# Kernel optimization log

Measured on AMD Instinct MI355X. Metric: run time of the kernel, lower is better.

## Reference

```python
import jax, jax.numpy as jnp
import numpy as np
from jax import lax

B, T, I, H = 64, 784, 1, 600


def setup_inputs() -> dict:
    key = jax.random.key(0)
    ks = jax.random.split(key, 9)
    k = 1.0 / np.sqrt(H)  # pytorch LSTMCell/Linear init scale
    x = jax.random.normal(ks[0], (B, T, I), dtype=jnp.float32)
    hs0 = jax.random.normal(ks[1], (B, H), dtype=jnp.float32)
    cs0 = jax.random.normal(ks[2], (B, H), dtype=jnp.float32)
    W_ih = jax.random.normal(ks[3], (4 * H, I), dtype=jnp.float32) * k
    W_hh = jax.random.normal(ks[4], (4 * H, H), dtype=jnp.float32) * k
    b_ih = jax.random.normal(ks[5], (4 * H,), dtype=jnp.float32) * k
    b_hh = jax.random.normal(ks[6], (4 * H,), dtype=jnp.float32) * k
    W_out = jax.random.normal(ks[7], (10, H), dtype=jnp.float32) * k
    b_out = jax.random.normal(ks[8], (10,), dtype=jnp.float32) * k
    return {"x": x, "hs0": hs0, "cs0": cs0, "W_ih": W_ih, "W_hh": W_hh,
            "b_ih": b_ih, "b_hh": b_hh, "W_out": W_out, "b_out": b_out}


def reference(x, hs0, cs0, W_ih, W_hh, b_ih, b_hh, W_out, b_out):
    # Precompute input projections for all timesteps in one GEMM: [B,T,4H]
    pre = jnp.einsum('bti,gi->btg', x, W_ih) + b_ih + b_hh
    pre_t = jnp.swapaxes(pre, 0, 1)  # [T,B,4H]

    def step(carry, p):
        h, c = carry
        gates = p + h @ W_hh.T  # [B,4H], pytorch gate order i,f,g,o
        i, f, g, o = jnp.split(gates, 4, axis=-1)
        c = jax.nn.sigmoid(f) * c + jax.nn.sigmoid(i) * jnp.tanh(g)
        h = jax.nn.sigmoid(o) * jnp.tanh(c)
        return (h, c), None

    (h, _), _ = lax.scan(step, (hs0, cs0), pre_t)
    return h @ W_out.T + b_out  # [B,10]
```

## Files before the change

kernel.cpp:

```cpp
#include <hip/hip_runtime.h>
#include <math.h>

#define BB 64
#define TT 784
#define HH 600
#define CG 50
#define SGN 4
#define CPW 12
#define BW 16
#define NWG (CG*SGN)
#define BLOCK 512
#define HB4 (BW*150)
#define LDS_BYTES (84*1024)

typedef float f2v __attribute__((ext_vector_type(2)));

__device__ __forceinline__ void ldg5_bypass(const float4* g0, const float4* g1,
                                            const float4* g2, const float4* g3,
                                            const float4* g4,
                                            float4& a, float4& b, float4& c,
                                            float4& d, float4& e) {
    asm volatile(
        "global_load_dwordx4 %0, %5, off sc0 sc1\n\t"
        "global_load_dwordx4 %1, %6, off sc0 sc1\n\t"
        "global_load_dwordx4 %2, %7, off sc0 sc1\n\t"
        "global_load_dwordx4 %3, %8, off sc0 sc1\n\t"
        "global_load_dwordx4 %4, %9, off sc0 sc1\n\t"
        "s_waitcnt vmcnt(0)"
        : "=&v"(a), "=&v"(b), "=&v"(c), "=&v"(d), "=&v"(e)
        : "v"(g0), "v"(g1), "v"(g2), "v"(g3), "v"(g4)
        : "memory");
}

__device__ __forceinline__ void stg_bypass(float* p, float v) {
    asm volatile("global_store_dword %0, %1, off sc0 sc1"
                 :: "v"(p), "v"(v) : "memory");
}

__device__ __forceinline__ float sigm_f(float v) {
    return 1.f / (1.f + __expf(-v));
}
__device__ __forceinline__ float tanh_f(float v) {
    return 1.f - 2.f / (__expf(2.f * v) + 1.f);
}

template<int MASK, int CNT>
__device__ __forceinline__ void fold(float* v, int kh) {
    const bool hi = (kh & MASK) != 0;
    #pragma unroll
    for (int i = 0; i < CNT; ++i) {
        float send = hi ? v[i] : v[i + CNT];
        float recv = __shfl_xor(send, MASK);
        v[i] = (hi ? v[i + CNT] : v[i]) + recv;
    }
}

extern "C" __global__ void __launch_bounds__(BLOCK, 2)
lstm_main(const float* __restrict__ x, const float* __restrict__ hs0,
          const float* __restrict__ cs0, const float* __restrict__ W_ih,
          const float* __restrict__ W_hh, const float* __restrict__ b_ih,
          const float* __restrict__ b_hh, float* __restrict__ hbuf,
          unsigned int* __restrict__ flags)
{
    extern __shared__ float lds[];
    float4* h4l  = (float4*)lds;
    float*  g_lds = lds + 4 * HB4;

    const int wg   = blockIdx.x;
    const int cg   = wg % CG;
    const int sg   = wg / CG;
    const int tid  = threadIdx.x;
    const int w    = tid >> 6;
    const int lane = tid & 63;
    const int bh   = lane >> 5;
    const int kh   = lane & 31;
    const int khc  = (kh < 30) ? kh : 29;
    const int b0   = sg * BW;

    f2v Wr2[6][10];
    #pragma unroll
    for (int r = 0; r < 6; ++r) {
        const int row = 6 * w + r;
        const int g   = row / 12, c = row % 12;
        const float* wrow = W_hh + ((size_t)g * HH + cg * CPW + c) * HH + khc * 20;
        #pragma unroll
        for (int j = 0; j < 5; ++j) {
            float4 t4 = (kh < 30) ? *(const float4*)(wrow + 4 * j)
                                  : make_float4(0.f, 0.f, 0.f, 0.f);
            Wr2[r][2 * j]     = (f2v){t4.x, t4.y};
            Wr2[r][2 * j + 1] = (f2v){t4.z, t4.w};
        }
    }

    float wihv[4], biasv[4], cst = 0.f;
    const int pc = tid >> 4, pb = tid & 15;
    const int cell = cg * CPW + pc;
    const int bglob = b0 + pb;
    if (tid < 192) {
        #pragma unroll
        for (int g = 0; g < 4; ++g) {
            const int grow = g * HH + cell;
            wihv[g]  = W_ih[grow];
            biasv[g] = b_ih[grow] + b_hh[grow];
        }
        cst = cs0[(size_t)bglob * HH + cell];
    }

    const int i0 = tid, i1 = tid + 512, i2 = tid + 1024, i3 = tid + 1536;
    const int i4 = (tid + 2048 < HB4) ? tid + 2048 : HB4 - 1;

    unsigned int* myflag = &flags[wg * 16];

    for (int t = 0; t < TT; ++t) {
        float xv = 0.f;
        if (tid < 192) xv = x[(size_t)bglob * TT + t];

        if (t > 0) {
            if (tid < CG) {
                const unsigned int* f = &flags[(sg * CG + tid) * 16];
                while (__hip_atomic_load(f, __ATOMIC_RELAXED,
                                         __HIP_MEMORY_SCOPE_AGENT) < (unsigned)t)
                    __builtin_amdgcn_s_sleep(1);
            }
        }
        __syncthreads();

        {
            const float* hsrc = (t == 0) ? hs0 : (hbuf + (size_t)(t & 1) * BB * HH);
            const float4* s4 = (const float4*)hsrc + (size_t)b0 * 150;
            float4 v0, v1, v2, v3, v4;
            ldg5_bypass(s4 + i0, s4 + i1, s4 + i2, s4 + i3, s4 + i4,
                        v0, v1, v2, v3, v4);
            h4l[i0] = v0; h4l[i1] = v1; h4l[i2] = v2; h4l[i3] = v3; h4l[i4] = v4;
        }
        __syncthreads();

        float v[48];
        {
            f2v acc2[6][8];
            #pragma unroll
            for (int r = 0; r < 6; ++r)
                #pragma unroll
                for (int bi = 0; bi < 8; ++bi)
                    acc2[r][bi] = (f2v){0.f, 0.f};

            const float4* hb_base = h4l + (size_t)bh * 8 * 150 + khc * 5;
            #pragma unroll
            for (int bi = 0; bi < 8; ++bi) {
                const float4* hb = hb_base + bi * 150;
                float4 hv[5];
                hv[0] = hb[0]; hv[1] = hb[1]; hv[2] = hb[2];
                hv[3] = hb[3]; hv[4] = hb[4];
                const f2v* h2 = (const f2v*)hv;
                #pragma unroll
                for (int r = 0; r < 6; ++r)
                    #pragma unroll
                    for (int j = 0; j < 10; ++j)
                        acc2[r][bi] = __builtin_elementwise_fma(Wr2[r][j],
                                                                h2[j],
                                                                acc2[r][bi]);
            }
            #pragma unroll
            for (int r = 0; r < 6; ++r)
                #pragma unroll
                for (int bi = 0; bi < 8; ++bi)
                    v[r * 8 + bi] = acc2[r][bi][0] + acc2[r][bi][1];
        }

        fold<16, 24>(v, kh);
        fold<8, 12>(v, kh);
        fold<4, 6>(v, kh);
        fold<2, 3>(v, kh);
        #pragma unroll
        for (int i = 0; i < 3; ++i)
            v[i] += __shfl_xor(v[i], 1);

        if (!(kh & 1)) {
            const int vb = 3 * (kh >> 1);
            #pragma unroll
            for (int s = 0; s < 3; ++s) {
                const int val = vb + s;
                const int rowl = val >> 3, bi = val & 7;
                g_lds[(6 * w + rowl) * 16 + bh * 8 + bi] = v[s];
            }
        }
        __syncthreads();

        float* hdst = hbuf + (size_t)((t + 1) & 1) * BB * HH;
        if (tid < 192) {
            const float gi = g_lds[(0 * 12 + pc) * 16 + pb] + xv * wihv[0] + biasv[0];
            const float gf = g_lds[(1 * 12 + pc) * 16 + pb] + xv * wihv[1] + biasv[1];
            const float gg = g_lds[(2 * 12 + pc) * 16 + pb] + xv * wihv[2] + biasv[2];
            const float go = g_lds[(3 * 12 + pc) * 16 + pb] + xv * wihv[3] + biasv[3];
            const float cn = sigm_f(gf) * cst + sigm_f(gi) * tanh_f(gg);
            cst = cn;
            stg_bypass(&hdst[(size_t)bglob * HH + cell], sigm_f(go) * tanh_f(cn));
        }
        asm volatile("s_waitcnt vmcnt(0)" ::: "memory");
        __syncthreads();
        if (tid == 0)
            __hip_atomic_store(myflag, (unsigned)(t + 1), __ATOMIC_RELAXED,
                               __HIP_MEMORY_SCOPE_AGENT);
    }
}

extern "C" __global__ void lstm_out(const float* __restrict__ hbuf0,
                                    const float* __restrict__ W_out,
                                    const float* __restrict__ b_out,
                                    float* __restrict__ out)
{
    int b = blockIdx.x;
    int lane = threadIdx.x;
    float acc[10] = {};
    for (int k = lane; k < HH; k += 64) {
        float hv = hbuf0[(size_t)b * HH + k];
        #pragma unroll
        for (int o = 0; o < 10; ++o)
            acc[o] += hv * W_out[(size_t)o * HH + k];
    }
    #pragma unroll
    for (int o = 0; o < 10; ++o) {
        float v = acc[o];
        for (int off = 32; off > 0; off >>= 1) v += __shfl_down(v, off);
        if (lane == 0) out[b * 10 + o] = v + b_out[o];
    }
}

extern "C" void kernel_launch(void* const* d_in, const int* in_sizes, int n_in,
                              void* d_out, int out_size, void* d_ws, size_t ws_size,
                              hipStream_t stream)
{
    const float* x     = (const float*)d_in[0];
    const float* hs0   = (const float*)d_in[1];
    const float* cs0   = (const float*)d_in[2];
    const float* W_ih  = (const float*)d_in[3];
    const float* W_hh  = (const float*)d_in[4];
    const float* b_ih  = (const float*)d_in[5];
    const float* b_hh  = (const float*)d_in[6];
    const float* W_out = (const float*)d_in[7];
    const float* b_out = (const float*)d_in[8];
    float* out = (float*)d_out;

    float* hbuf = (float*)d_ws;
    unsigned int* flags = (unsigned int*)((char*)d_ws + (size_t)2 * BB * HH * sizeof(float));

    hipFuncSetAttribute((const void*)lstm_main,
                        hipFuncAttributeMaxDynamicSharedMemorySize, LDS_BYTES);

    hipMemsetAsync(flags, 0, NWG * 16 * sizeof(unsigned int), stream);
    hipLaunchKernelGGL(lstm_main, dim3(NWG), dim3(BLOCK), LDS_BYTES, stream,
                       x, hs0, cs0, W_ih, W_hh, b_ih, b_hh, hbuf, flags);
    hipLaunchKernelGGL(lstm_out, dim3(BB), dim3(64), 0, stream,
                       hbuf, W_out, b_out, out);
}
```

Measured before the change: 4.499 ms.

## Split K across waves with per-wave flag polling and async global-to-LDS h chunks

Moves W_hh from registers into LDS and splits the hidden dimension across the 8 waves. Each wave waits only on the producer workgroups whose h columns it consumes, then streams those chunks straight into LDS with global_load_lds and computes as each chunk lands. The shuffle-based reduction tree is replaced by LDS atomicAdd into the gate buffer. Flags become counters bumped by three waves per step, which removes the block-wide wait before the whole-h copy. The cost is more LDS traffic for weights, LDS atomic contention, and a lower occupancy hint.

```diff
diff --git a/kernel.cpp b/kernel.cpp
--- a/kernel.cpp
+++ b/kernel.cpp
@@ -5,31 +5,22 @@
 #define TT 784
 #define HH 600
 #define CG 50
-#define SGN 4
 #define CPW 12
 #define BW 16
-#define NWG (CG*SGN)
+#define NWG (CG*4)
 #define BLOCK 512
-#define HB4 (BW*150)
-#define LDS_BYTES (84*1024)
+#define WSTR 612
+#define CBUF_DW 192
+#define NBUF 7
+#define LDS_BYTES ((48*WSTR + 8*NBUF*CBUF_DW + 48*16)*4)
 
 typedef float f2v __attribute__((ext_vector_type(2)));
 
-__device__ __forceinline__ void ldg5_bypass(const float4* g0, const float4* g1,
-                                            const float4* g2, const float4* g3,
-                                            const float4* g4,
-                                            float4& a, float4& b, float4& c,
-                                            float4& d, float4& e) {
-    asm volatile(
-        "global_load_dwordx4 %0, %5, off sc0 sc1\n\t"
-        "global_load_dwordx4 %1, %6, off sc0 sc1\n\t"
-        "global_load_dwordx4 %2, %7, off sc0 sc1\n\t"
-        "global_load_dwordx4 %3, %8, off sc0 sc1\n\t"
-        "global_load_dwordx4 %4, %9, off sc0 sc1\n\t"
-        "s_waitcnt vmcnt(0)"
-        : "=&v"(a), "=&v"(b), "=&v"(c), "=&v"(d), "=&v"(e)
-        : "v"(g0), "v"(g1), "v"(g2), "v"(g3), "v"(g4)
-        : "memory");
+__device__ __forceinline__ float sigm_f(float v) {
+    return 1.f / (1.f + __expf(-v));
+}
+__device__ __forceinline__ float tanh_f(float v) {
+    return 1.f - 2.f / (__expf(2.f * v) + 1.f);
 }
 
 __device__ __forceinline__ void stg_bypass(float* p, float v) {
@@ -37,25 +28,43 @@
                  :: "v"(p), "v"(v) : "memory");
 }
 
-__device__ __forceinline__ float sigm_f(float v) {
-    return 1.f / (1.f + __expf(-v));
-}
-__device__ __forceinline__ float tanh_f(float v) {
-    return 1.f - 2.f / (__expf(2.f * v) + 1.f);
-}
-
-template<int MASK, int CNT>
-__device__ __forceinline__ void fold(float* v, int kh) {
-    const bool hi = (kh & MASK) != 0;
+template<int NCH>
+__device__ __forceinline__ void process_chunks(const float* __restrict__ W_lds,
+                                               const float* __restrict__ mycbuf,
+                                               int nst, int rt, int bt,
+                                               f2v (&acc2)[3][4])
+{
     #pragma unroll
-    for (int i = 0; i < CNT; ++i) {
-        float send = hi ? v[i] : v[i + CNT];
-        float recv = __shfl_xor(send, MASK);
-        v[i] = (hi ? v[i + CNT] : v[i]) + recv;
-    }
-}
-
-extern "C" __global__ void __launch_bounds__(BLOCK, 2)
+    for (int i = 0; i < NCH; ++i) {
+        asm volatile("s_waitcnt vmcnt(%c0)" :: "n"(NCH - 1 - i) : "memory");
+        __builtin_amdgcn_sched_barrier(0);
+        const float* cb = mycbuf + i * CBUF_DW;
+        float4 hv[4][3];
+        #pragma unroll
+        for (int jj = 0; jj < 4; ++jj)
+            #pragma unroll
+            for (int jc = 0; jc < 3; ++jc)
+                hv[jj][jc] = *(const float4*)&cb[(3 * (4 * bt + jj) + jc) * 4];
+        const int p = nst + i;
+        #pragma unroll
+        for (int ii = 0; ii < 3; ++ii) {
+            const float* wrow = W_lds + (3 * rt + ii) * WSTR + 12 * p;
+            #pragma unroll
+            for (int jc = 0; jc < 3; ++jc) {
+                float4 wv = *(const float4*)&wrow[4 * jc];
+                const f2v* w2 = (const f2v*)&wv;
+                #pragma unroll
+                for (int jj = 0; jj < 4; ++jj) {
+                    const f2v* h2 = (const f2v*)&hv[jj][jc];
+                    acc2[ii][jj] = __builtin_elementwise_fma(w2[0], h2[0], acc2[ii][jj]);
+                    acc2[ii][jj] = __builtin_elementwise_fma(w2[1], h2[1], acc2[ii][jj]);
+                }
+            }
+        }
+    }
+}
+
+extern "C" __global__ void __launch_bounds__(BLOCK)
 lstm_main(const float* __restrict__ x, const float* __restrict__ hs0,
           const float* __restrict__ cs0, const float* __restrict__ W_ih,
           const float* __restrict__ W_hh, const float* __restrict__ b_ih,
@@ -63,8 +72,9 @@
           unsigned int* __restrict__ flags)
 {
     extern __shared__ float lds[];
-    float4* h4l  = (float4*)lds;
-    float*  g_lds = lds + 4 * HB4;
+    float* W_lds = lds;
+    float* cbuf  = lds + 48 * WSTR;
+    float* g_lds = lds + 48 * WSTR + 8 * NBUF * CBUF_DW;
 
     const int wg   = blockIdx.x;
     const int cg   = wg % CG;
@@ -72,30 +82,26 @@
     const int tid  = threadIdx.x;
     const int w    = tid >> 6;
     const int lane = tid & 63;
-    const int bh   = lane >> 5;
-    const int kh   = lane & 31;
-    const int khc  = (kh < 30) ? kh : 29;
+    const int rt   = lane >> 2;
+    const int bt   = lane & 3;
     const int b0   = sg * BW;
-
-    f2v Wr2[6][10];
-    #pragma unroll
-    for (int r = 0; r < 6; ++r) {
-        const int row = 6 * w + r;
-        const int g   = row / 12, c = row % 12;
-        const float* wrow = W_hh + ((size_t)g * HH + cg * CPW + c) * HH + khc * 20;
-        #pragma unroll
-        for (int j = 0; j < 5; ++j) {
-            float4 t4 = (kh < 30) ? *(const float4*)(wrow + 4 * j)
-                                  : make_float4(0.f, 0.f, 0.f, 0.f);
-            Wr2[r][2 * j]     = (f2v){t4.x, t4.y};
-            Wr2[r][2 * j + 1] = (f2v){t4.z, t4.w};
-        }
-    }
-
-    float wihv[4], biasv[4], cst = 0.f;
+    const int nst  = (25 * w) >> 2;
+    const int nen  = (25 * (w + 1)) >> 2;
+    const int nch  = nen - nst;
+    const int sb   = lane / 3, sj = lane - 3 * sb;
+    float* mycbuf  = cbuf + w * NBUF * CBUF_DW;
+
+    for (int i4 = tid; i4 < 48 * 150; i4 += BLOCK) {
+        int r = i4 / 150, col = i4 - r * 150;
+        int gg = r / 12, cc = r - gg * 12;
+        *(float4*)&W_lds[r * WSTR + 4 * col] =
+            *(const float4*)(W_hh + ((size_t)(gg * HH + cg * CPW + cc)) * HH + 4 * col);
+    }
+
     const int pc = tid >> 4, pb = tid & 15;
     const int cell = cg * CPW + pc;
     const int bglob = b0 + pb;
+    float wihv[4], biasv[4], cst = 0.f;
     if (tid < 192) {
         #pragma unroll
         for (int g = 0; g < 4; ++g) {
@@ -106,101 +112,65 @@
         cst = cs0[(size_t)bglob * HH + cell];
     }
 
-    const int i0 = tid, i1 = tid + 512, i2 = tid + 1024, i3 = tid + 1536;
-    const int i4 = (tid + 2048 < HB4) ? tid + 2048 : HB4 - 1;
-
     unsigned int* myflag = &flags[wg * 16];
+    const unsigned int* pollp =
+        &flags[(sg * CG + nst + ((lane < nch) ? lane : 0)) * 16];
+    const bool mine = (lane < nch);
 
     for (int t = 0; t < TT; ++t) {
-        float xv = 0.f;
-        if (tid < 192) xv = x[(size_t)bglob * TT + t];
+        if (tid < 192) *(float4*)&g_lds[4 * tid] = make_float4(0.f, 0.f, 0.f, 0.f);
+        __syncthreads();
 
         if (t > 0) {
-            if (tid < CG) {
-                const unsigned int* f = &flags[(sg * CG + tid) * 16];
-                while (__hip_atomic_load(f, __ATOMIC_RELAXED,
-                                         __HIP_MEMORY_SCOPE_AGENT) < (unsigned)t)
-                    __builtin_amdgcn_s_sleep(1);
+            const unsigned thr3 = 3u * (unsigned)t;
+            for (;;) {
+                unsigned fv = __hip_atomic_load(pollp, __ATOMIC_RELAXED,
+                                                __HIP_MEMORY_SCOPE_AGENT);
+                if (__all(!mine || fv >= thr3)) break;
+                __builtin_amdgcn_s_sleep(1);
             }
         }
+        const float* hsrc = (t == 0) ? hs0 : (hbuf + (size_t)(t & 1) * BB * HH);
+        for (int i = 0; i < nch; ++i) {
+            if (lane < 48) {
+                const float* gp = hsrc + (size_t)(b0 + sb) * HH
+                                       + 12 * (nst + i) + 4 * sj;
+                __builtin_amdgcn_global_load_lds(gp, (void*)(mycbuf + i * CBUF_DW),
+                                                 16, 0, 17 );
+            }
+        }
+        f2v acc2[3][4];
+        #pragma unroll
+        for (int ii = 0; ii < 3; ++ii)
+            #pragma unroll
+            for (int jj = 0; jj < 4; ++jj)
+                acc2[ii][jj] = (f2v){0.f, 0.f};
+        if (nch == 7) process_chunks<7>(W_lds, mycbuf, nst, rt, bt, acc2);
+        else          process_chunks<6>(W_lds, mycbuf, nst, rt, bt, acc2);
+
+        #pragma unroll
+        for (int ii = 0; ii < 3; ++ii)
+            #pragma unroll
+            for (int jj = 0; jj < 4; ++jj)
+                atomicAdd(&g_lds[(3 * rt + ii) * 16 + 4 * bt + jj],
+                          acc2[ii][jj][0] + acc2[ii][jj][1]);
         __syncthreads();
 
-        {
-            const float* hsrc = (t == 0) ? hs0 : (hbuf + (size_t)(t & 1) * BB * HH);
-            const float4* s4 = (const float4*)hsrc + (size_t)b0 * 150;
-            float4 v0, v1, v2, v3, v4;
-            ldg5_bypass(s4 + i0, s4 + i1, s4 + i2, s4 + i3, s4 + i4,
-                        v0, v1, v2, v3, v4);
-            h4l[i0] = v0; h4l[i1] = v1; h4l[i2] = v2; h4l[i3] = v3; h4l[i4] = v4;
+        if (tid < 192) {
+            const float xv = x[(size_t)bglob * TT + t];
+            const float gi  = g_lds[(0 * CPW + pc) * 16 + pb] + xv * wihv[0] + biasv[0];
+            const float gf  = g_lds[(1 * CPW + pc) * 16 + pb] + xv * wihv[1] + biasv[1];
+            const float gg_ = g_lds[(2 * CPW + pc) * 16 + pb] + xv * wihv[2] + biasv[2];
+            const float go  = g_lds[(3 * CPW + pc) * 16 + pb] + xv * wihv[3] + biasv[3];
+            const float cn = sigm_f(gf) * cst + sigm_f(gi) * tanh_f(gg_);
+            cst = cn;
+            const float hv = sigm_f(go) * tanh_f(cn);
+            stg_bypass(hbuf + (size_t)((t + 1) & 1) * BB * HH
+                            + (size_t)bglob * HH + cell, hv);
+            asm volatile("s_waitcnt vmcnt(0)" ::: "memory");
+            if (lane == 0) atomicAdd(myflag, 1u);
         }
         __syncthreads();
-
-        float v[48];
-        {
-            f2v acc2[6][8];
-            #pragma unroll
-            for (int r = 0; r < 6; ++r)
-                #pragma unroll
-                for (int bi = 0; bi < 8; ++bi)
-                    acc2[r][bi] = (f2v){0.f, 0.f};
-
-            const float4* hb_base = h4l + (size_t)bh * 8 * 150 + khc * 5;
-            #pragma unroll
-            for (int bi = 0; bi < 8; ++bi) {
-                const float4* hb = hb_base + bi * 150;
-                float4 hv[5];
-                hv[0] = hb[0]; hv[1] = hb[1]; hv[2] = hb[2];
-                hv[3] = hb[3]; hv[4] = hb[4];
-                const f2v* h2 = (const f2v*)hv;
-                #pragma unroll
-                for (int r = 0; r < 6; ++r)
-                    #pragma unroll
-                    for (int j = 0; j < 10; ++j)
-                        acc2[r][bi] = __builtin_elementwise_fma(Wr2[r][j],
-                                                                h2[j],
-                                                                acc2[r][bi]);
-            }
-            #pragma unroll
-            for (int r = 0; r < 6; ++r)
-                #pragma unroll
-                for (int bi = 0; bi < 8; ++bi)
-                    v[r * 8 + bi] = acc2[r][bi][0] + acc2[r][bi][1];
-        }
-
-        fold<16, 24>(v, kh);
-        fold<8, 12>(v, kh);
-        fold<4, 6>(v, kh);
-        fold<2, 3>(v, kh);
-        #pragma unroll
-        for (int i = 0; i < 3; ++i)
-            v[i] += __shfl_xor(v[i], 1);
-
-        if (!(kh & 1)) {
-            const int vb = 3 * (kh >> 1);
-            #pragma unroll
-            for (int s = 0; s < 3; ++s) {
-                const int val = vb + s;
-                const int rowl = val >> 3, bi = val & 7;
-                g_lds[(6 * w + rowl) * 16 + bh * 8 + bi] = v[s];
-            }
-        }
-        __syncthreads();
-
-        float* hdst = hbuf + (size_t)((t + 1) & 1) * BB * HH;
-        if (tid < 192) {
-            const float gi = g_lds[(0 * 12 + pc) * 16 + pb] + xv * wihv[0] + biasv[0];
-            const float gf = g_lds[(1 * 12 + pc) * 16 + pb] + xv * wihv[1] + biasv[1];
-            const float gg = g_lds[(2 * 12 + pc) * 16 + pb] + xv * wihv[2] + biasv[2];
-            const float go = g_lds[(3 * 12 + pc) * 16 + pb] + xv * wihv[3] + biasv[3];
-            const float cn = sigm_f(gf) * cst + sigm_f(gi) * tanh_f(gg);
-            cst = cn;
-            stg_bypass(&hdst[(size_t)bglob * HH + cell], sigm_f(go) * tanh_f(cn));
-        }
-        asm volatile("s_waitcnt vmcnt(0)" ::: "memory");
-        __syncthreads();
-        if (tid == 0)
-            __hip_atomic_store(myflag, (unsigned)(t + 1), __ATOMIC_RELAXED,
-                               __HIP_MEMORY_SCOPE_AGENT);
     }
 }
 
```

Result: slower. 10.64 ms (+136.6%).
